# Performance work log

Measured on AMD Instinct MI355X. Metric: run time of the kernel, lower is better.

The kernel has to match this reference:

```python
import jax, jax.numpy as jnp
import numpy as np

N_NODES = 1_000_000
N_EDGES = 16_000_000
BATCH = 1_000_000
EMBED_DIM = 3


def setup_inputs() -> dict:
    key = jax.random.key(0)
    ks = jax.random.split(key, 11)
    edge_index = jax.random.randint(ks[0], (2, N_EDGES), 0, N_NODES, dtype=jnp.int32)
    edge_weight = jax.random.uniform(ks[1], (N_EDGES,), dtype=jnp.float32) + 0.1
    home = jax.random.randint(ks[2], (BATCH,), 0, N_NODES, dtype=jnp.int32)
    away = jax.random.randint(ks[3], (BATCH,), 0, N_NODES, dtype=jnp.int32)
    emb = jax.random.normal(ks[4], (N_NODES, EMBED_DIM), dtype=jnp.float32)
    w_conv = jax.random.normal(ks[5], (3, 3), dtype=jnp.float32) * 0.5
    b_conv = jax.random.normal(ks[6], (3,), dtype=jnp.float32) * 0.1
    w1 = jax.random.normal(ks[7], (6, 6), dtype=jnp.float32) * 0.4
    b1 = jax.random.normal(ks[8], (6,), dtype=jnp.float32) * 0.1
    w3 = jax.random.normal(ks[9], (6, 3), dtype=jnp.float32) * 0.4
    b3 = jax.random.normal(ks[10], (3,), dtype=jnp.float32) * 0.1
    return {"edge_index": edge_index, "edge_weight": edge_weight, "home": home,
            "away": away, "emb": emb, "w_conv": w_conv, "b_conv": b_conv,
            "w1": w1, "b1": b1, "w3": w3, "b3": b3}


def reference(edge_index, edge_weight, home, away, emb, w_conv, b_conv, w1, b1, w3, b3):
    n = emb.shape[0]
    row, col = edge_index[0], edge_index[1]
    # gcn_norm (symmetric, add_self_loops=False): deg over target nodes
    deg = jax.ops.segment_sum(edge_weight, col, num_segments=n)
    dinv = jnp.where(deg > 0, jax.lax.rsqrt(jnp.where(deg > 0, deg, 1.0)), 0.0)
    norm = dinv[row] * edge_weight * dinv[col]  # [E]
    x = emb @ w_conv                            # [N,3] transformed features
    msg = norm[:, None] * x[row]                # [E,3] gather + scale
    agg = jax.ops.segment_sum(msg, col, num_segments=n) + b_conv  # [N,3]
    x = jax.nn.leaky_relu(agg)                  # conv1 output
    h = jnp.concatenate([x[home], x[away]], axis=-1)  # [B,6]
    h = jax.nn.leaky_relu(h @ w1 + b1)          # lin1
    h = jax.nn.leaky_relu(h @ w3 + b3)          # lin3 -> [B,3]
    return jax.nn.log_softmax(h, axis=0)        # LogSoftmax over dim=0 as in source
```

## Files before the change

### kernel.cpp

```cpp
#include <hip/hip_runtime.h>
#include <math.h>

#define NN 1000000
#define NE 16000000
#define NB 1000000
#define NEQ (NE / 4)
#define BN 4096
#define NBUCK 245
#define NBUCKR 256
#define NBLK 1024
#define CMASK 0xFFFFFu

__device__ __forceinline__ float leaky(float v) { return v > 0.f ? v : 0.01f * v; }

__device__ __forceinline__ void atomicMaxF(float* addr, float val) {
    unsigned int* ia = (unsigned int*)addr;
    unsigned int old = *ia;
    while (true) {
        float f = __uint_as_float(old);
        if (f >= val) break;
        unsigned int prev = atomicCAS(ia, old, __float_as_uint(val));
        if (prev == old) break;
        old = prev;
    }
}

__global__ void init_stats(float* stats) {
    int t = threadIdx.x;
    if (t < 3) stats[t] = -1e30f;
    else if (t < 6) stats[t] = 0.f;
}

__global__ __launch_bounds__(256) void count_kernel(const int4* __restrict__ col4,
                                                    unsigned int* __restrict__ HG) {
    __shared__ unsigned int h[NBUCKR];
    h[threadIdx.x] = 0u;
    __syncthreads();
    int stride = gridDim.x * 256;
    for (int i = blockIdx.x * 256 + threadIdx.x; i < NEQ; i += stride) {
        int4 c = col4[i];
        atomicAdd(&h[((unsigned int)c.x) >> 12], 1u);
        atomicAdd(&h[((unsigned int)c.y) >> 12], 1u);
        atomicAdd(&h[((unsigned int)c.z) >> 12], 1u);
        atomicAdd(&h[((unsigned int)c.w) >> 12], 1u);
    }
    __syncthreads();
    HG[(size_t)threadIdx.x * NBLK + blockIdx.x] = h[threadIdx.x];
}

__global__ __launch_bounds__(256) void scan_sum(const unsigned int* __restrict__ HG,
                                                unsigned int* __restrict__ part) {
    const unsigned int* p = HG + (size_t)blockIdx.x * NBLK;
    unsigned int s = 0;
    for (int i = threadIdx.x; i < NBLK; i += 256) s += p[i];
    #pragma unroll
    for (int off = 32; off > 0; off >>= 1) s += __shfl_down(s, off);
    __shared__ unsigned int sm[4];
    int wave = threadIdx.x >> 6, lane = threadIdx.x & 63;
    if (lane == 0) sm[wave] = s;
    __syncthreads();
    if (threadIdx.x == 0) part[blockIdx.x] = sm[0] + sm[1] + sm[2] + sm[3];
}

__global__ void scan_part(unsigned int* part) {
    __shared__ unsigned int tmp[256];
    int t = threadIdx.x;
    unsigned int v = part[t];
    tmp[t] = v;
    __syncthreads();
    for (int off = 1; off < 256; off <<= 1) {
        unsigned int add = (t >= off) ? tmp[t - off] : 0u;
        __syncthreads();
        tmp[t] += add;
        __syncthreads();
    }
    part[t] = tmp[t] - v;
}

__global__ __launch_bounds__(256) void scan_apply(unsigned int* __restrict__ HG,
                                                  const unsigned int* __restrict__ part) {
    __shared__ unsigned int vals[NBLK];
    __shared__ unsigned int ts[256];
    int t = threadIdx.x;
    unsigned int* p = HG + (size_t)blockIdx.x * NBLK;
    for (int i = t; i < NBLK; i += 256) vals[i] = p[i];
    __syncthreads();
    unsigned int a0 = vals[4 * t], a1 = vals[4 * t + 1], a2 = vals[4 * t + 2], a3 = vals[4 * t + 3];
    unsigned int ls = a0 + a1 + a2 + a3;
    ts[t] = ls;
    __syncthreads();
    for (int off = 1; off < 256; off <<= 1) {
        unsigned int add = (t >= off) ? ts[t - off] : 0u;
        __syncthreads();
        ts[t] += add;
        __syncthreads();
    }
    unsigned int base = part[blockIdx.x] + ts[t] - ls;
    p[4 * t] = base;
    p[4 * t + 1] = base + a0;
    p[4 * t + 2] = base + a0 + a1;
    p[4 * t + 3] = base + a0 + a1 + a2;
}

__global__ __launch_bounds__(256) void scatter_kernel(const int4* __restrict__ row4,
                                                      const int4* __restrict__ col4,
                                                      const float4* __restrict__ w4,
                                                      const unsigned int* __restrict__ HG,
                                                      uint2* __restrict__ rec) {
    __shared__ unsigned int pos[NBUCKR];
    pos[threadIdx.x] = HG[(size_t)threadIdx.x * NBLK + blockIdx.x];
    __syncthreads();
    int stride = gridDim.x * 256;
    for (int i = blockIdx.x * 256 + threadIdx.x; i < NEQ; i += stride) {
        int4 r = row4[i];
        int4 c = col4[i];
        float4 w = w4[i];
        {
            unsigned int cu = (unsigned int)c.x;
            unsigned int p = atomicAdd(&pos[cu >> 12], 1u);
            rec[p] = make_uint2((unsigned int)r.x | ((cu & 4095u) << 20), __float_as_uint(w.x));
        }
        {
            unsigned int cu = (unsigned int)c.y;
            unsigned int p = atomicAdd(&pos[cu >> 12], 1u);
            rec[p] = make_uint2((unsigned int)r.y | ((cu & 4095u) << 20), __float_as_uint(w.y));
        }
        {
            unsigned int cu = (unsigned int)c.z;
            unsigned int p = atomicAdd(&pos[cu >> 12], 1u);
            rec[p] = make_uint2((unsigned int)r.z | ((cu & 4095u) << 20), __float_as_uint(w.z));
        }
        {
            unsigned int cu = (unsigned int)c.w;
            unsigned int p = atomicAdd(&pos[cu >> 12], 1u);
            rec[p] = make_uint2((unsigned int)r.w | ((cu & 4095u) << 20), __float_as_uint(w.w));
        }
    }
}

__global__ __launch_bounds__(512) void bucket_deg_kernel(const uint2* __restrict__ rec,
                                                         const unsigned int* __restrict__ HG,
                                                         const float* __restrict__ emb,
                                                         const float* __restrict__ w_conv,
                                                         float* __restrict__ dinv,
                                                         float4* __restrict__ y) {
    __shared__ float degl[BN];
    int b = blockIdx.x;
    for (int t = threadIdx.x; t < BN; t += 512) degl[t] = 0.f;
    unsigned int s = HG[(size_t)b * NBLK];
    unsigned int e = HG[(size_t)(b + 1) * NBLK];
    __syncthreads();
    unsigned int i = s + threadIdx.x;
    for (; i + 1536 < e; i += 2048) {
        uint2 r0 = rec[i], r1 = rec[i + 512], r2 = rec[i + 1024], r3 = rec[i + 1536];
        atomicAdd(&degl[r0.x >> 20], __uint_as_float(r0.y));
        atomicAdd(&degl[r1.x >> 20], __uint_as_float(r1.y));
        atomicAdd(&degl[r2.x >> 20], __uint_as_float(r2.y));
        atomicAdd(&degl[r3.x >> 20], __uint_as_float(r3.y));
    }
    for (; i < e; i += 512) {
        uint2 r0 = rec[i];
        atomicAdd(&degl[r0.x >> 20], __uint_as_float(r0.y));
    }
    __syncthreads();
    float wc[9];
    #pragma unroll
    for (int k = 0; k < 9; k++) wc[k] = w_conv[k];
    int node0 = b * BN;
    for (int t = threadIdx.x; t < BN; t += 512) {
        int g = node0 + t;
        if (g >= NN) break;
        float d = degl[t];
        float di = d > 0.f ? rsqrtf(d) : 0.f;
        dinv[g] = di;
        float e0 = emb[3 * g], e1 = emb[3 * g + 1], e2 = emb[3 * g + 2];
        float x0 = e0 * wc[0] + e1 * wc[3] + e2 * wc[6];
        float x1 = e0 * wc[1] + e1 * wc[4] + e2 * wc[7];
        float x2 = e0 * wc[2] + e1 * wc[5] + e2 * wc[8];
        y[g] = make_float4(di * x0, di * x1, di * x2, 0.f);
    }
}

__global__ __launch_bounds__(512) void bucket_agg_kernel(const uint2* __restrict__ rec,
                                                         const unsigned int* __restrict__ HG,
                                                         const float4* __restrict__ y,
                                                         const float* __restrict__ dinv,
                                                         const float* __restrict__ b_conv,
                                                         float4* __restrict__ xf) {
    __shared__ float acc[BN * 3];
    int b = blockIdx.x;
    for (int t = threadIdx.x; t < BN * 3; t += 512) acc[t] = 0.f;
    unsigned int s = HG[(size_t)b * NBLK];
    unsigned int e = HG[(size_t)(b + 1) * NBLK];
    __syncthreads();
    unsigned int i = s + threadIdx.x;
    for (; i + 1536 < e; i += 2048) {
        uint2 r0 = rec[i], r1 = rec[i + 512], r2 = rec[i + 1024], r3 = rec[i + 1536];
        float4 y0 = y[r0.x & CMASK];
        float4 y1 = y[r1.x & CMASK];
        float4 y2 = y[r2.x & CMASK];
        float4 y3 = y[r3.x & CMASK];
        float w0 = __uint_as_float(r0.y), w1 = __uint_as_float(r1.y);
        float w2 = __uint_as_float(r2.y), w3 = __uint_as_float(r3.y);
        unsigned int c0 = (r0.x >> 20) * 3, c1 = (r1.x >> 20) * 3;
        unsigned int c2 = (r2.x >> 20) * 3, c3 = (r3.x >> 20) * 3;
        atomicAdd(&acc[c0 + 0], w0 * y0.x); atomicAdd(&acc[c0 + 1], w0 * y0.y); atomicAdd(&acc[c0 + 2], w0 * y0.z);
        atomicAdd(&acc[c1 + 0], w1 * y1.x); atomicAdd(&acc[c1 + 1], w1 * y1.y); atomicAdd(&acc[c1 + 2], w1 * y1.z);
        atomicAdd(&acc[c2 + 0], w2 * y2.x); atomicAdd(&acc[c2 + 1], w2 * y2.y); atomicAdd(&acc[c2 + 2], w2 * y2.z);
        atomicAdd(&acc[c3 + 0], w3 * y3.x); atomicAdd(&acc[c3 + 1], w3 * y3.y); atomicAdd(&acc[c3 + 2], w3 * y3.z);
    }
    for (; i < e; i += 512) {
        uint2 r0 = rec[i];
        float4 y0 = y[r0.x & CMASK];
        float w0 = __uint_as_float(r0.y);
        unsigned int c0 = (r0.x >> 20) * 3;
        atomicAdd(&acc[c0 + 0], w0 * y0.x); atomicAdd(&acc[c0 + 1], w0 * y0.y); atomicAdd(&acc[c0 + 2], w0 * y0.z);
    }
    __syncthreads();
    float bc0 = b_conv[0], bc1 = b_conv[1], bc2 = b_conv[2];
    int node0 = b * BN;
    for (int t = threadIdx.x; t < BN; t += 512) {
        int g = node0 + t;
        if (g >= NN) break;
        float di = dinv[g];
        xf[g] = make_float4(leaky(di * acc[3 * t + 0] + bc0),
                            leaky(di * acc[3 * t + 1] + bc1),
                            leaky(di * acc[3 * t + 2] + bc2), 0.f);
    }
}

__global__ __launch_bounds__(256) void batch_kernel(const int4* __restrict__ home4,
                                                    const int4* __restrict__ away4,
                                                    const float4* __restrict__ xf,
                                                    const float* __restrict__ w1,
                                                    const float* __restrict__ b1,
                                                    const float* __restrict__ w3,
                                                    const float* __restrict__ b3,
                                                    float4* __restrict__ out4,
                                                    float* __restrict__ stats, int nq) {
    int i = blockIdx.x * blockDim.x + threadIdx.x;
    float m0 = -1e30f, m1 = -1e30f, m2 = -1e30f;
    if (i < nq) {
        float W1[36], B1[6], W3[18], B3[3];
        #pragma unroll
        for (int k = 0; k < 36; k++) W1[k] = w1[k];
        #pragma unroll
        for (int k = 0; k < 6; k++) B1[k] = b1[k];
        #pragma unroll
        for (int k = 0; k < 18; k++) W3[k] = w3[k];
        #pragma unroll
        for (int k = 0; k < 3; k++) B3[k] = b3[k];

        int4 hh = home4[i], aa = away4[i];
        int hs[4] = {hh.x, hh.y, hh.z, hh.w};
        int as_[4] = {aa.x, aa.y, aa.z, aa.w};
        float o[12];
        #pragma unroll
        for (int e = 0; e < 4; e++) {
            float4 xh = xf[hs[e]];
            float4 xa = xf[as_[e]];
            float h[6] = {xh.x, xh.y, xh.z, xa.x, xa.y, xa.z};
            float l1v[6];
            #pragma unroll
            for (int j = 0; j < 6; j++) {
                float s = B1[j];
                #pragma unroll
                for (int k = 0; k < 6; k++) s += h[k] * W1[k * 6 + j];
                l1v[j] = leaky(s);
            }
            float o3[3];
            #pragma unroll
            for (int j = 0; j < 3; j++) {
                float s = B3[j];
                #pragma unroll
                for (int k = 0; k < 6; k++) s += l1v[k] * W3[k * 3 + j];
                o3[j] = leaky(s);
            }
            o[3 * e + 0] = o3[0];
            o[3 * e + 1] = o3[1];
            o[3 * e + 2] = o3[2];
            m0 = fmaxf(m0, o3[0]);
            m1 = fmaxf(m1, o3[1]);
            m2 = fmaxf(m2, o3[2]);
        }
        #pragma unroll
        for (int q = 0; q < 3; q++)
            out4[3 * (size_t)i + q] = make_float4(o[4 * q], o[4 * q + 1], o[4 * q + 2], o[4 * q + 3]);
    }
    #pragma unroll
    for (int off = 32; off > 0; off >>= 1) {
        m0 = fmaxf(m0, __shfl_down(m0, off));
        m1 = fmaxf(m1, __shfl_down(m1, off));
        m2 = fmaxf(m2, __shfl_down(m2, off));
    }
    __shared__ float sm[3][4];
    int wave = threadIdx.x >> 6, lane = threadIdx.x & 63;
    if (lane == 0) { sm[0][wave] = m0; sm[1][wave] = m1; sm[2][wave] = m2; }
    __syncthreads();
    if (threadIdx.x == 0) {
        atomicMaxF(&stats[0], fmaxf(fmaxf(sm[0][0], sm[0][1]), fmaxf(sm[0][2], sm[0][3])));
        atomicMaxF(&stats[1], fmaxf(fmaxf(sm[1][0], sm[1][1]), fmaxf(sm[1][2], sm[1][3])));
        atomicMaxF(&stats[2], fmaxf(fmaxf(sm[2][0], sm[2][1]), fmaxf(sm[2][2], sm[2][3])));
    }
}

__global__ __launch_bounds__(256) void sumexp_kernel(const float4* __restrict__ out4,
                                                     float* __restrict__ stats, int nq) {
    float mx0 = stats[0], mx1 = stats[1], mx2 = stats[2];
    int i = blockIdx.x * blockDim.x + threadIdx.x;
    float s0 = 0.f, s1 = 0.f, s2 = 0.f;
    if (i < nq) {
        float4 v = out4[i];
        float vals[4] = {v.x, v.y, v.z, v.w};
        int c = (4 * i) % 3;
        #pragma unroll
        for (int e = 0; e < 4; e++) {
            float mv = (c == 0) ? mx0 : ((c == 1) ? mx1 : mx2);
            float ee = expf(vals[e] - mv);
            if (c == 0) s0 += ee; else if (c == 1) s1 += ee; else s2 += ee;
            c = (c == 2) ? 0 : (c + 1);
        }
    }
    #pragma unroll
    for (int off = 32; off > 0; off >>= 1) {
        s0 += __shfl_down(s0, off);
        s1 += __shfl_down(s1, off);
        s2 += __shfl_down(s2, off);
    }
    __shared__ float sm[3][4];
    int wave = threadIdx.x >> 6, lane = threadIdx.x & 63;
    if (lane == 0) { sm[0][wave] = s0; sm[1][wave] = s1; sm[2][wave] = s2; }
    __syncthreads();
    if (threadIdx.x == 0) {
        atomicAdd(&stats[3], sm[0][0] + sm[0][1] + sm[0][2] + sm[0][3]);
        atomicAdd(&stats[4], sm[1][0] + sm[1][1] + sm[1][2] + sm[1][3]);
        atomicAdd(&stats[5], sm[2][0] + sm[2][1] + sm[2][2] + sm[2][3]);
    }
}

__global__ __launch_bounds__(256) void final_kernel(float4* __restrict__ out4,
                                                    const float* __restrict__ stats, int nq) {
    float o0 = stats[0] + logf(stats[3]);
    float o1 = stats[1] + logf(stats[4]);
    float o2 = stats[2] + logf(stats[5]);
    int i = blockIdx.x * blockDim.x + threadIdx.x;
    if (i >= nq) return;
    float4 v = out4[i];
    float vals[4] = {v.x, v.y, v.z, v.w};
    int c = (4 * i) % 3;
    #pragma unroll
    for (int e = 0; e < 4; e++) {
        vals[e] -= (c == 0) ? o0 : ((c == 1) ? o1 : o2);
        c = (c == 2) ? 0 : (c + 1);
    }
    out4[i] = make_float4(vals[0], vals[1], vals[2], vals[3]);
}

extern "C" void kernel_launch(void* const* d_in, const int* in_sizes, int n_in,
                              void* d_out, int out_size, void* d_ws, size_t ws_size,
                              hipStream_t stream) {
    const int*   edge_index  = (const int*)d_in[0];
    const float* edge_weight = (const float*)d_in[1];
    const int*   home        = (const int*)d_in[2];
    const int*   away        = (const int*)d_in[3];
    const float* emb         = (const float*)d_in[4];
    const float* w_conv      = (const float*)d_in[5];
    const float* b_conv      = (const float*)d_in[6];
    const float* w1          = (const float*)d_in[7];
    const float* b1          = (const float*)d_in[8];
    const float* w3          = (const float*)d_in[9];
    const float* b3          = (const float*)d_in[10];
    float* out = (float*)d_out;

    char* ws = (char*)d_ws;
    uint2*        rec   = (uint2*)(ws);
    unsigned int* HG    = (unsigned int*)(ws + 128000000);
    unsigned int* part  = (unsigned int*)(ws + 129048576);
    float*        dinv  = (float*)(ws + 129049600);
    float4*       y     = (float4*)(ws + 133049600);
    float4*       xf    = (float4*)(ws + 149049600);
    float*        stats = (float*)(ws + 165049600);

    const int* row = edge_index;
    const int* col = edge_index + NE;

    init_stats<<<1, 64, 0, stream>>>(stats);

    count_kernel<<<NBLK, 256, 0, stream>>>((const int4*)col, HG);
    scan_sum<<<NBUCKR, 256, 0, stream>>>(HG, part);
    scan_part<<<1, 256, 0, stream>>>(part);
    scan_apply<<<NBUCKR, 256, 0, stream>>>(HG, part);
    scatter_kernel<<<NBLK, 256, 0, stream>>>((const int4*)row, (const int4*)col,
                                             (const float4*)edge_weight, HG, rec);

    bucket_deg_kernel<<<NBUCK, 512, 0, stream>>>(rec, HG, emb, w_conv, dinv, y);
    bucket_agg_kernel<<<NBUCK, 512, 0, stream>>>(rec, HG, y, dinv, b_conv, xf);

    const int BQ = NB / 4;
    const int OQ = (NB * 3) / 4;
    batch_kernel<<<(BQ + 255) / 256, 256, 0, stream>>>((const int4*)home, (const int4*)away, xf,
                                                       w1, b1, w3, b3, (float4*)out, stats, BQ);
    sumexp_kernel<<<(OQ + 255) / 256, 256, 0, stream>>>((const float4*)out, stats, OQ);
    final_kernel<<<(OQ + 255) / 256, 256, 0, stream>>>((float4*)out, stats, OQ);
}
```

Before: 913.5 us.

## Split bucket edge ranges across more blocks and store node features as fp16

The degree and aggregation bucket kernels now split each bucket's edge range four ways, so there are four times as many blocks. Each block flushes its shared-memory partial sums to global buffers with atomics, and separate per-node kernels finish the normalisation, transform and activation. The gathered node features y and xf are packed into half precision (8 bytes instead of 16) to cut random-gather traffic. The cost is two extra kernels, two memsets, global atomic flushes, and some precision loss in the intermediate features.

```diff
diff --git a/kernel.cpp b/kernel.cpp
--- a/kernel.cpp
+++ b/kernel.cpp
@@ -1,4 +1,5 @@
 #include <hip/hip_runtime.h>
+#include <hip/hip_fp16.h>
 #include <math.h>
 
 #define NN 1000000
@@ -9,9 +10,26 @@
 #define NBUCK 245
 #define NBUCKR 256
 #define NBLK 1024
+#define SSPLIT 4
 #define CMASK 0xFFFFFu
 
 __device__ __forceinline__ float leaky(float v) { return v > 0.f ? v : 0.01f * v; }
+
+__device__ __forceinline__ uint2 pack_h4(float x, float y, float z) {
+    __half2 a = __floats2half2_rn(x, y);
+    __half2 b = __floats2half2_rn(z, 0.f);
+    uint2 u;
+    u.x = *(unsigned int*)&a;
+    u.y = *(unsigned int*)&b;
+    return u;
+}
+
+__device__ __forceinline__ float3 unpack_h4(uint2 u) {
+    __half2 a = *(__half2*)&u.x;
+    __half2 b = *(__half2*)&u.y;
+    float2 fa = __half22float2(a);
+    return make_float3(fa.x, fa.y, __low2float(b));
+}
 
 __device__ __forceinline__ void atomicMaxF(float* addr, float val) {
     unsigned int* ia = (unsigned int*)addr;
@@ -140,66 +158,76 @@
 
 __global__ __launch_bounds__(512) void bucket_deg_kernel(const uint2* __restrict__ rec,
                                                          const unsigned int* __restrict__ HG,
-                                                         const float* __restrict__ emb,
-                                                         const float* __restrict__ w_conv,
-                                                         float* __restrict__ dinv,
-                                                         float4* __restrict__ y) {
+                                                         float* __restrict__ deg_g) {
     __shared__ float degl[BN];
-    int b = blockIdx.x;
+    int b = blockIdx.x % NBUCK;
+    int sp = blockIdx.x / NBUCK;
     for (int t = threadIdx.x; t < BN; t += 512) degl[t] = 0.f;
-    unsigned int s = HG[(size_t)b * NBLK];
-    unsigned int e = HG[(size_t)(b + 1) * NBLK];
-    __syncthreads();
-    unsigned int i = s + threadIdx.x;
-    for (; i + 1536 < e; i += 2048) {
+    unsigned int s0 = HG[(size_t)b * NBLK];
+    unsigned int e0 = HG[(size_t)(b + 1) * NBLK];
+    unsigned int n = e0 - s0;
+    unsigned int beg = s0 + (unsigned int)((unsigned long long)n * sp / SSPLIT);
+    unsigned int end = s0 + (unsigned int)((unsigned long long)n * (sp + 1) / SSPLIT);
+    __syncthreads();
+    unsigned int i = beg + threadIdx.x;
+    for (; i + 1536 < end; i += 2048) {
         uint2 r0 = rec[i], r1 = rec[i + 512], r2 = rec[i + 1024], r3 = rec[i + 1536];
         atomicAdd(&degl[r0.x >> 20], __uint_as_float(r0.y));
         atomicAdd(&degl[r1.x >> 20], __uint_as_float(r1.y));
         atomicAdd(&degl[r2.x >> 20], __uint_as_float(r2.y));
         atomicAdd(&degl[r3.x >> 20], __uint_as_float(r3.y));
     }
-    for (; i < e; i += 512) {
+    for (; i < end; i += 512) {
         uint2 r0 = rec[i];
         atomicAdd(&degl[r0.x >> 20], __uint_as_float(r0.y));
     }
     __syncthreads();
-    float wc[9];
-    #pragma unroll
-    for (int k = 0; k < 9; k++) wc[k] = w_conv[k];
     int node0 = b * BN;
     for (int t = threadIdx.x; t < BN; t += 512) {
-        int g = node0 + t;
-        if (g >= NN) break;
-        float d = degl[t];
-        float di = d > 0.f ? rsqrtf(d) : 0.f;
-        dinv[g] = di;
-        float e0 = emb[3 * g], e1 = emb[3 * g + 1], e2 = emb[3 * g + 2];
-        float x0 = e0 * wc[0] + e1 * wc[3] + e2 * wc[6];
-        float x1 = e0 * wc[1] + e1 * wc[4] + e2 * wc[7];
-        float x2 = e0 * wc[2] + e1 * wc[5] + e2 * wc[8];
-        y[g] = make_float4(di * x0, di * x1, di * x2, 0.f);
-    }
+        float v = degl[t];
+        if (v != 0.f) atomicAdd(&deg_g[node0 + t], v);
+    }
+}
+
+__global__ __launch_bounds__(256) void node1_kernel(const float* __restrict__ deg_g,
+                                                    const float* __restrict__ emb,
+                                                    const float* __restrict__ w_conv,
+                                                    float* __restrict__ dinv,
+                                                    uint2* __restrict__ y) {
+    int g = blockIdx.x * 256 + threadIdx.x;
+    if (g >= NN) return;
+    float d = deg_g[g];
+    float di = d > 0.f ? rsqrtf(d) : 0.f;
+    dinv[g] = di;
+    float e0 = emb[3 * g], e1 = emb[3 * g + 1], e2 = emb[3 * g + 2];
+    float x0 = e0 * w_conv[0] + e1 * w_conv[3] + e2 * w_conv[6];
+    float x1 = e0 * w_conv[1] + e1 * w_conv[4] + e2 * w_conv[7];
+    float x2 = e0 * w_conv[2] + e1 * w_conv[5] + e2 * w_conv[8];
+    y[g] = pack_h4(di * x0, di * x1, di * x2);
 }
 
 __global__ __launch_bounds__(512) void bucket_agg_kernel(const uint2* __restrict__ rec,
                                                          const unsigned int* __restrict__ HG,
-                                                         const float4* __restrict__ y,
-                                                         const float* __restrict__ dinv,
-                                                         const float* __restrict__ b_conv,
-                                                         float4* __restrict__ xf) {
+                                                         const uint2* __restrict__ y,
+                                                         float* __restrict__ acc_g) {
     __shared__ float acc[BN * 3];
-    int b = blockIdx.x;
+    int b = blockIdx.x % NBUCK;
+    int sp = blockIdx.x / NBUCK;
     for (int t = threadIdx.x; t < BN * 3; t += 512) acc[t] = 0.f;
-    unsigned int s = HG[(size_t)b * NBLK];
-    unsigned int e = HG[(size_t)(b + 1) * NBLK];
-    __syncthreads();
-    unsigned int i = s + threadIdx.x;
-    for (; i + 1536 < e; i += 2048) {
+    unsigned int s0 = HG[(size_t)b * NBLK];
+    unsigned int e0 = HG[(size_t)(b + 1) * NBLK];
+    unsigned int n = e0 - s0;
+    unsigned int beg = s0 + (unsigned int)((unsigned long long)n * sp / SSPLIT);
+    unsigned int end = s0 + (unsigned int)((unsigned long long)n * (sp + 1) / SSPLIT);
+    __syncthreads();
+    unsigned int i = beg + threadIdx.x;
+    for (; i + 1536 < end; i += 2048) {
         uint2 r0 = rec[i], r1 = rec[i + 512], r2 = rec[i + 1024], r3 = rec[i + 1536];
-        float4 y0 = y[r0.x & CMASK];
-        float4 y1 = y[r1.x & CMASK];
-        float4 y2 = y[r2.x & CMASK];
-        float4 y3 = y[r3.x & CMASK];
+        uint2 u0 = y[r0.x & CMASK];
+        uint2 u1 = y[r1.x & CMASK];
+        uint2 u2 = y[r2.x & CMASK];
+        uint2 u3 = y[r3.x & CMASK];
+        float3 y0 = unpack_h4(u0), y1 = unpack_h4(u1), y2 = unpack_h4(u2), y3 = unpack_h4(u3);
         float w0 = __uint_as_float(r0.y), w1 = __uint_as_float(r1.y);
         float w2 = __uint_as_float(r2.y), w3 = __uint_as_float(r3.y);
         unsigned int c0 = (r0.x >> 20) * 3, c1 = (r1.x >> 20) * 3;
@@ -209,29 +237,37 @@
         atomicAdd(&acc[c2 + 0], w2 * y2.x); atomicAdd(&acc[c2 + 1], w2 * y2.y); atomicAdd(&acc[c2 + 2], w2 * y2.z);
         atomicAdd(&acc[c3 + 0], w3 * y3.x); atomicAdd(&acc[c3 + 1], w3 * y3.y); atomicAdd(&acc[c3 + 2], w3 * y3.z);
     }
-    for (; i < e; i += 512) {
+    for (; i < end; i += 512) {
         uint2 r0 = rec[i];
-        float4 y0 = y[r0.x & CMASK];
+        float3 y0 = unpack_h4(y[r0.x & CMASK]);
         float w0 = __uint_as_float(r0.y);
         unsigned int c0 = (r0.x >> 20) * 3;
         atomicAdd(&acc[c0 + 0], w0 * y0.x); atomicAdd(&acc[c0 + 1], w0 * y0.y); atomicAdd(&acc[c0 + 2], w0 * y0.z);
     }
     __syncthreads();
-    float bc0 = b_conv[0], bc1 = b_conv[1], bc2 = b_conv[2];
-    int node0 = b * BN;
-    for (int t = threadIdx.x; t < BN; t += 512) {
-        int g = node0 + t;
-        if (g >= NN) break;
-        float di = dinv[g];
-        xf[g] = make_float4(leaky(di * acc[3 * t + 0] + bc0),
-                            leaky(di * acc[3 * t + 1] + bc1),
-                            leaky(di * acc[3 * t + 2] + bc2), 0.f);
-    }
+    size_t base = (size_t)b * BN * 3;
+    for (int t = threadIdx.x; t < BN * 3; t += 512) {
+        float v = acc[t];
+        if (v != 0.f) atomicAdd(&acc_g[base + t], v);
+    }
+}
+
+__global__ __launch_bounds__(256) void node2_kernel(const float* __restrict__ acc_g,
+                                                    const float* __restrict__ dinv,
+                                                    const float* __restrict__ b_conv,
+                                                    uint2* __restrict__ xf) {
+    int g = blockIdx.x * 256 + threadIdx.x;
+    if (g >= NN) return;
+    float di = dinv[g];
+    float a0 = acc_g[3 * (size_t)g], a1 = acc_g[3 * (size_t)g + 1], a2 = acc_g[3 * (size_t)g + 2];
+    xf[g] = pack_h4(leaky(di * a0 + b_conv[0]),
+                    leaky(di * a1 + b_conv[1]),
+                    leaky(di * a2 + b_conv[2]));
 }
 
 __global__ __launch_bounds__(256) void batch_kernel(const int4* __restrict__ home4,
                                                     const int4* __restrict__ away4,
-                                                    const float4* __restrict__ xf,
+                                                    const uint2* __restrict__ xf,
                                                     const float* __restrict__ w1,
                                                     const float* __restrict__ b1,
                                                     const float* __restrict__ w3,
@@ -257,8 +293,8 @@
         float o[12];
         #pragma unroll
         for (int e = 0; e < 4; e++) {
-            float4 xh = xf[hs[e]];
-            float4 xa = xf[as_[e]];
+            float3 xh = unpack_h4(xf[hs[e]]);
+            float3 xa = unpack_h4(xf[as_[e]]);
             float h[6] = {xh.x, xh.y, xh.z, xa.x, xa.y, xa.z};
             float l1v[6];
             #pragma unroll
@@ -376,15 +412,19 @@
     uint2*        rec   = (uint2*)(ws);
     unsigned int* HG    = (unsigned int*)(ws + 128000000);
     unsigned int* part  = (unsigned int*)(ws + 129048576);
-    float*        dinv  = (float*)(ws + 129049600);
-    float4*       y     = (float4*)(ws + 133049600);
-    float4*       xf    = (float4*)(ws + 149049600);
-    float*        stats = (float*)(ws + 165049600);
+    float*        deg_g = (float*)(ws + 129049600);
+    float*        dinv  = (float*)(ws + 133063680);
+    uint2*        y     = (uint2*)(ws + 137063680);
+    float*        acc_g = (float*)(ws + 145063680);
+    uint2*        xf    = (uint2*)(ws + 157105920);
+    float*        stats = (float*)(ws + 165105920);
 
     const int* row = edge_index;
     const int* col = edge_index + NE;
 
     init_stats<<<1, 64, 0, stream>>>(stats);
+    hipMemsetAsync(deg_g, 0, 4014080, stream);
+    hipMemsetAsync(acc_g, 0, 12042240, stream);
 
     count_kernel<<<NBLK, 256, 0, stream>>>((const int4*)col, HG);
     scan_sum<<<NBUCKR, 256, 0, stream>>>(HG, part);
@@ -393,8 +433,10 @@
     scatter_kernel<<<NBLK, 256, 0, stream>>>((const int4*)row, (const int4*)col,
                                              (const float4*)edge_weight, HG, rec);
 
-    bucket_deg_kernel<<<NBUCK, 512, 0, stream>>>(rec, HG, emb, w_conv, dinv, y);
-    bucket_agg_kernel<<<NBUCK, 512, 0, stream>>>(rec, HG, y, dinv, b_conv, xf);
+    bucket_deg_kernel<<<NBUCK * SSPLIT, 512, 0, stream>>>(rec, HG, deg_g);
+    node1_kernel<<<(NN + 255) / 256, 256, 0, stream>>>(deg_g, emb, w_conv, dinv, y);
+    bucket_agg_kernel<<<NBUCK * SSPLIT, 512, 0, stream>>>(rec, HG, y, acc_g);
+    node2_kernel<<<(NN + 255) / 256, 256, 0, stream>>>(acc_g, dinv, b_conv, xf);
 
     const int BQ = NB / 4;
     const int OQ = (NB * 3) / 4;
```

Measured after the change: 929.0 us. Within noise of the previous version (+1.7%).
